# Kernel optimization log

Measured on AMD Instinct MI355X. Metric: run time of the kernel, lower is better.

Reference implementation:

```python
import jax, jax.numpy as jnp
import numpy as np

VOCAB, D, L, HEADS, MAX_T = 32000, 1024, 6, 16, 2048
HD = D // HEADS
DFF = 4 * D
B, T = 2, 2048
EPS = 1e-5


def setup_inputs() -> dict:
    key = jax.random.key(0)
    ks = jax.random.split(key, 16)
    s = 0.02
    return {
        "ids": jax.random.randint(ks[0], (B, T), 0, VOCAB, dtype=jnp.int32),
        "emb": jax.random.normal(ks[1], (VOCAB, D), jnp.float32) * s,
        "pos": jax.random.normal(ks[2], (MAX_T, D), jnp.float32) * s,
        "ln1_g": jnp.ones((L, D), jnp.float32),
        "ln1_b": jnp.zeros((L, D), jnp.float32),
        "ln2_g": jnp.ones((L, D), jnp.float32),
        "ln2_b": jnp.zeros((L, D), jnp.float32),
        "qkv_w": jax.random.normal(ks[3], (L, 3 * D, D), jnp.float32) * s,
        "out_w": jax.random.normal(ks[4], (L, D, D), jnp.float32) * s,
        "mlp_w1": jax.random.normal(ks[5], (L, DFF, D), jnp.float32) * s,
        "mlp_b1": jnp.zeros((L, DFF), jnp.float32),
        "mlp_w2": jax.random.normal(ks[6], (L, D, DFF), jnp.float32) * s,
        "mlp_b2": jnp.zeros((L, D), jnp.float32),
        "lnf_g": jnp.ones((D,), jnp.float32),
        "lnf_b": jnp.zeros((D,), jnp.float32),
    }


def layernorm(x, g, b):
    mu = jnp.mean(x, axis=-1, keepdims=True)
    var = jnp.mean(jnp.square(x - mu), axis=-1, keepdims=True)
    return (x - mu) * jax.lax.rsqrt(var + EPS) * g + b


def attention(x, qkv_w, out_w):
    b, t, d = x.shape
    qkv = jnp.einsum('btd,ed->bte', x, qkv_w)  # [B,T,3D]
    qkv = qkv.reshape(b, t, 3, HEADS, HD)
    q, k, v = qkv[:, :, 0], qkv[:, :, 1], qkv[:, :, 2]  # [B,T,H,hd]
    scale = HD ** -0.5
    scores = jnp.einsum('bqhd,bkhd->bhqk', q, k) * scale
    causal = jnp.tril(jnp.ones((t, t), dtype=bool))
    scores = jnp.where(causal, scores, -jnp.inf)
    attn = jax.nn.softmax(scores, axis=-1)
    o = jnp.einsum('bhqk,bkhd->bqhd', attn, v).reshape(b, t, d)
    return jnp.einsum('btd,ed->bte', o, out_w)


def reference(ids, emb, pos, ln1_g, ln1_b, ln2_g, ln2_b, qkv_w, out_w,
              mlp_w1, mlp_b1, mlp_w2, mlp_b2, lnf_g, lnf_b):
    t = ids.shape[1]
    x = emb[ids] + pos[:t][None, :, :]
    for l in range(L):
        x = x + attention(layernorm(x, ln1_g[l], ln1_b[l]), qkv_w[l], out_w[l])
        h = layernorm(x, ln2_g[l], ln2_b[l])
        h = jax.nn.gelu(jnp.einsum('btd,fd->btf', h, mlp_w1[l]) + mlp_b1[l], approximate=False)
        x = x + jnp.einsum('btf,df->btd', h, mlp_w2[l]) + mlp_b2[l]
    x = layernorm(x, lnf_g, lnf_b)
    return jnp.einsum('btd,vd->btv', x, emb)  # tied head
```

## Files before the change

kernel.cpp:

```cpp
#include <hip/hip_runtime.h>
#include <math.h>

#define TSEQ   2048
#define BATCH  2
#define DMODEL 1024
#define NLAYER 6
#define NHEAD  16
#define HDIM   64
#define DFFN   4096
#define NVOCAB 32000
#define LNEPS  1e-5f

typedef __bf16 bf16_t;
typedef bf16_t bf16x8 __attribute__((ext_vector_type(8)));
typedef float  f32x4  __attribute__((ext_vector_type(4)));
typedef unsigned short u16;
typedef u16 u16x4 __attribute__((ext_vector_type(4)));
typedef u16 u16x8 __attribute__((ext_vector_type(8)));

#define GBAR()   __builtin_amdgcn_s_barrier()
#define WLGKM0() asm volatile("s_waitcnt lgkmcnt(0)" ::: "memory")
#define WVM4()   asm volatile("s_waitcnt vmcnt(4)" ::: "memory")
#define WVM2()   asm volatile("s_waitcnt vmcnt(2)" ::: "memory")
#define WVM0()   asm volatile("s_waitcnt vmcnt(0)" ::: "memory")

__device__ __forceinline__ u16 f2bf(float f) {
  unsigned u = __float_as_uint(f);
  return (u16)((u + 0x7fffu + ((u >> 16) & 1u)) >> 16);
}

__device__ __forceinline__ void gload16(const void* g, void* l) {
  __builtin_amdgcn_global_load_lds(
      (const __attribute__((address_space(1))) unsigned int*)g,
      (__attribute__((address_space(3))) unsigned int*)l, 16, 0, 0);
}

__global__ __launch_bounds__(256) void embed_kernel(
    const int* __restrict__ ids, const float* __restrict__ emb,
    const float* __restrict__ pos, float* __restrict__ x) {
  int bt  = blockIdx.x;
  int t   = bt & (TSEQ - 1);
  int id  = ids[bt];
  int tid = threadIdx.x;
  float4 e = ((const float4*)(emb + (size_t)id * DMODEL))[tid];
  float4 p = ((const float4*)(pos + (size_t)t  * DMODEL))[tid];
  float4 r;
  r.x = e.x + p.x; r.y = e.y + p.y; r.z = e.z + p.z; r.w = e.w + p.w;
  ((float4*)(x + (size_t)bt * DMODEL))[tid] = r;
}

__device__ __forceinline__ void ln_body(
    const float* __restrict__ x, const float* __restrict__ g,
    const float* __restrict__ b, u16* __restrict__ y, int row, float* red) {
  int tid = threadIdx.x;
  int lane = tid & 63, w = tid >> 6;
  float4 v = ((const float4*)(x + (size_t)row * DMODEL))[tid];
  float s = v.x + v.y + v.z + v.w;
#pragma unroll
  for (int o = 32; o >= 1; o >>= 1) s += __shfl_xor(s, o);
  if (lane == 0) red[w] = s;
  __syncthreads();
  float mu = (red[0] + red[1] + red[2] + red[3]) * (1.0f / DMODEL);
  float d0 = v.x - mu, d1 = v.y - mu, d2 = v.z - mu, d3 = v.w - mu;
  float s2 = d0*d0 + d1*d1 + d2*d2 + d3*d3;
#pragma unroll
  for (int o = 32; o >= 1; o >>= 1) s2 += __shfl_xor(s2, o);
  if (lane == 0) red[4 + w] = s2;
  __syncthreads();
  float var = (red[4] + red[5] + red[6] + red[7]) * (1.0f / DMODEL);
  float rs = rsqrtf(var + LNEPS);
  float4 gv = ((const float4*)g)[tid];
  float4 bv = ((const float4*)b)[tid];
  u16x4 r;
  r[0] = f2bf(d0 * rs * gv.x + bv.x);
  r[1] = f2bf(d1 * rs * gv.y + bv.y);
  r[2] = f2bf(d2 * rs * gv.z + bv.z);
  r[3] = f2bf(d3 * rs * gv.w + bv.w);
  ((u16x4*)(y + (size_t)row * DMODEL))[tid] = r;
}

__global__ __launch_bounds__(256) void ln_kernel(
    const float* __restrict__ x, const float* __restrict__ g,
    const float* __restrict__ b, u16* __restrict__ y) {
  __shared__ float red[8];
  ln_body(x, g, b, y, blockIdx.x, red);
}

__device__ __forceinline__ void cvt8_body(const float* src, u16* dst, size_t i) {
  f32x4 a = __builtin_nontemporal_load((const f32x4*)(src + i));
  f32x4 b = __builtin_nontemporal_load((const f32x4*)(src + i) + 1);
  u16x8 r;
  r[0] = f2bf(a[0]); r[1] = f2bf(a[1]); r[2] = f2bf(a[2]); r[3] = f2bf(a[3]);
  r[4] = f2bf(b[0]); r[5] = f2bf(b[1]); r[6] = f2bf(b[2]); r[7] = f2bf(b[3]);
  *(u16x8*)(dst + i) = r;
}

__global__ __launch_bounds__(256) void prep_kernel(
    const float* __restrict__ s0, const float* __restrict__ s1,
    const float* __restrict__ s2, const float* __restrict__ s3,
    u16* __restrict__ d0, u16* __restrict__ d1,
    u16* __restrict__ d2, u16* __restrict__ d3,
    const float* __restrict__ x, const float* __restrict__ g,
    const float* __restrict__ b, u16* __restrict__ y) {
  __shared__ float red[8];
  int bid = blockIdx.x;
  if (bid >= 6144) {
    ln_body(x, g, b, y, bid - 6144, red);
    return;
  }
  const float* src; u16* dst; int idx;
  if (bid < 1536)      { src = s0; dst = d0; idx = bid; }
  else if (bid < 2048) { src = s1; dst = d1; idx = bid - 1536; }
  else if (bid < 4096) { src = s2; dst = d2; idx = bid - 2048; }
  else                 { src = s3; dst = d3; idx = bid - 4096; }
  cvt8_body(src, dst, ((size_t)idx * 256 + threadIdx.x) * 8);
}

__global__ __launch_bounds__(256) void finprep_kernel(
    const float* __restrict__ x, const float* __restrict__ g,
    const float* __restrict__ b, u16* __restrict__ y,
    const float* __restrict__ emb, u16* __restrict__ embb) {
  __shared__ float red[8];
  int bid = blockIdx.x;
  if (bid < 4096) {
    ln_body(x, g, b, y, bid, red);
    return;
  }
  cvt8_body(emb, embb, ((size_t)(bid - 4096) * 256 + threadIdx.x) * 8);
}

__device__ __forceinline__ float gelu_f(float v) {
  return 0.5f * v * (1.0f + erff(v * 0.70710678118654752f));
}

__device__ __forceinline__ bf16x8 ldsrd(const char* p) {
  return *(const bf16x8*)p;
}

template<int QD>
__device__ __forceinline__ void rd_a(bf16x8 (&afr)[2][2], const char* base,
                                     int aB0, int aB1) {
  afr[0][0] = ldsrd(base + aB0 + QD * 4096);
  afr[0][1] = ldsrd(base + aB1 + QD * 4096);
  afr[1][0] = ldsrd(base + aB0 + QD * 4096 + 2048);
  afr[1][1] = ldsrd(base + aB1 + QD * 4096 + 2048);
}

__device__ __forceinline__ void rd_b(bf16x8 (&bfr)[4][2], const char* base,
                                     int bB0, int bB1) {
#pragma unroll
  for (int ni = 0; ni < 4; ++ni) {
    bfr[ni][0] = ldsrd(base + bB0 + ni * 2048);
    bfr[ni][1] = ldsrd(base + bB1 + ni * 2048);
  }
}

template<int QD>
__device__ __forceinline__ void mm16(f32x4 (&acc)[8][4], bf16x8 (&afr)[2][2],
                                     bf16x8 (&bfr)[4][2]) {
#pragma unroll
  for (int ni = 0; ni < 4; ++ni) {
    acc[QD*2+0][ni] = __builtin_amdgcn_mfma_f32_16x16x32_bf16(bfr[ni][0], afr[0][0], acc[QD*2+0][ni], 0, 0, 0);
    acc[QD*2+0][ni] = __builtin_amdgcn_mfma_f32_16x16x32_bf16(bfr[ni][1], afr[0][1], acc[QD*2+0][ni], 0, 0, 0);
    acc[QD*2+1][ni] = __builtin_amdgcn_mfma_f32_16x16x32_bf16(bfr[ni][0], afr[1][0], acc[QD*2+1][ni], 0, 0, 0);
    acc[QD*2+1][ni] = __builtin_amdgcn_mfma_f32_16x16x32_bf16(bfr[ni][1], afr[1][1], acc[QD*2+1][ni], 0, 0, 0);
  }
}

template<int ACT, bool BIAS, bool OUTBF, bool NTB>
__global__ __launch_bounds__(512, 2) void gemm_mfma256(
    const bf16_t* __restrict__ A, const bf16_t* __restrict__ W,
    const float* __restrict__ bias, void* __restrict__ Cout,
    int M, int N, int K) {
  __shared__ char lds[131072];
  char* Asc = lds;
  char* Bsc = lds + 65536;

  const int tid  = threadIdx.x;
  const int lane = tid & 63;
  const int w    = tid >> 6;
  const int wr   = w >> 2, wc = w & 3;

  const int nwg = gridDim.x * gridDim.y;
  const int bid = blockIdx.y * gridDim.x + blockIdx.x;
  const int swz = (bid & 7) * (nwg >> 3) + (bid >> 3);
  const int m0 = (swz & 15) << 8;
  const int n0 = (swz >> 4) << 8;

  const size_t K2 = (size_t)K * 2;
  const int KT = K >> 6;

  const int qsrc = (((tid & 7) ^ ((tid >> 3) & 7)) << 4);
  const char* srcA = (const char*)A + (size_t)(m0 + (tid >> 3)) * K2 + qsrc;
  const char* srcB = (const char*)W + (size_t)(n0 + (tid >> 3)) * K2 + qsrc;
  char* dstA = Asc + (tid & 448) * 16;
  char* dstB = Bsc + (tid & 448) * 16;

  auto STG = [&](int kt, int part) {
    if (kt >= KT) return;
    const int h = part & 1;
    const size_t so = (size_t)(h * 128) * K2 + (size_t)kt * 128;
    const int dofs = ((kt & 1) << 15) + (h << 14);
    if (part >= 2) {
      gload16(srcA + so, dstA + dofs);
      gload16(srcA + so + 64 * K2, dstA + dofs + 8192);
    } else {
      gload16(srcB + so, dstB + dofs);
      gload16(srcB + so + 64 * K2, dstB + dofs + 8192);
    }
  };

  const int rr = lane & 15;
  const int q0 = (((lane >> 4) ^ (lane & 7)) << 4);
  const int aB0 = ((wr << 7) + rr) * 128 + q0;
  const int aB1 = ((wr << 7) + rr) * 128 + (q0 ^ 64);
  const int bB0 = ((wc << 6) + rr) * 128 + q0;
  const int bB1 = ((wc << 6) + rr) * 128 + (q0 ^ 64);

  bf16x8 bfr[4][2];
  bf16x8 afr[2][2];
  f32x4 acc[8][4] = {};

  STG(0, 0); STG(0, 1); STG(0, 2); STG(0, 3);
  STG(1, 0); STG(1, 1);
  WVM4();
  GBAR();

  const int iters = KT >> 1;
  for (int t = 0; t < iters; ++t) {
    const int d = t << 1;
    rd_b(bfr, Bsc, bB0, bB1);
    rd_a<0>(afr, Asc, aB0, aB1);
    STG(d + 1, 2); STG(d + 1, 3);
    GBAR(); WLGKM0();
    __builtin_amdgcn_s_setprio(1); mm16<0>(acc, afr, bfr); __builtin_amdgcn_s_setprio(0);
    GBAR();
    rd_a<1>(afr, Asc, aB0, aB1);
    STG(d + 2, 0);
    GBAR(); WLGKM0();
    __builtin_amdgcn_s_setprio(1); mm16<1>(acc, afr, bfr); __builtin_amdgcn_s_setprio(0);
    GBAR();
    rd_a<2>(afr, Asc, aB0, aB1);
    STG(d + 2, 1);
    GBAR(); WLGKM0();
    __builtin_amdgcn_s_setprio(1); mm16<2>(acc, afr, bfr); __builtin_amdgcn_s_setprio(0);
    GBAR();
    rd_a<3>(afr, Asc, aB0, aB1);
    GBAR(); WLGKM0();
    __builtin_amdgcn_s_setprio(1); mm16<3>(acc, afr, bfr); __builtin_amdgcn_s_setprio(0);
    if (t == iters - 1) { WVM0(); } else { WVM4(); }
    GBAR();
    rd_b(bfr, Bsc + 32768, bB0, bB1);
    rd_a<0>(afr, Asc + 32768, aB0, aB1);
    STG(d + 2, 2);
    GBAR(); WLGKM0();
    __builtin_amdgcn_s_setprio(1); mm16<0>(acc, afr, bfr); __builtin_amdgcn_s_setprio(0);
    GBAR();
    rd_a<1>(afr, Asc + 32768, aB0, aB1);
    STG(d + 2, 3);
    GBAR(); WLGKM0();
    __builtin_amdgcn_s_setprio(1); mm16<1>(acc, afr, bfr); __builtin_amdgcn_s_setprio(0);
    GBAR();
    rd_a<2>(afr, Asc + 32768, aB0, aB1);
    STG(d + 3, 0);
    GBAR(); WLGKM0();
    __builtin_amdgcn_s_setprio(1); mm16<2>(acc, afr, bfr); __builtin_amdgcn_s_setprio(0);
    GBAR();
    rd_a<3>(afr, Asc + 32768, aB0, aB1);
    STG(d + 3, 1);
    GBAR(); WLGKM0();
    __builtin_amdgcn_s_setprio(1); mm16<3>(acc, afr, bfr); __builtin_amdgcn_s_setprio(0);
    WVM4();
    GBAR();
  }

  const int cc = lane & 15;
  const int jb = (lane >> 4) << 2;

  if (NTB) {
    float* lbuf = (float*)lds;
#pragma unroll
    for (int h = 0; h < 2; ++h) {
      if (h) GBAR();
#pragma unroll
      for (int mi4 = 0; mi4 < 4; ++mi4) {
        const int lr = wr * 64 + mi4 * 16 + cc;
#pragma unroll
        for (int ni = 0; ni < 4; ++ni) {
          const int colb = (wc * 64 + ni * 16 + jb) * 4;
          f32x4 v = acc[h * 4 + mi4][ni];
          if (BIAS) v += *(const f32x4*)(bias + n0 + wc * 64 + ni * 16 + jb);
          if (ACT == 1) {
#pragma unroll
            for (int j = 0; j < 4; ++j) v[j] = gelu_f(v[j]);
          }
          *(f32x4*)((char*)lbuf + lr * 1024 + (colb ^ ((lr & 7) << 4))) = v;
        }
      }
      GBAR();
#pragma unroll
      for (int r = 0; r < 16; ++r) {
        const int lr = w * 16 + r;
        const int grow = m0 + h * 64 + lr + ((lr >> 6) << 6);
        const int cb = (lane * 16) ^ ((lr & 7) << 4);
        f32x4 v = *(const f32x4*)((const char*)lbuf + lr * 1024 + cb);
        __builtin_nontemporal_store(
            v, (f32x4*)((char*)((float*)Cout + (size_t)grow * N + n0) + lane * 16));
      }
    }
    return;
  }

  const int orow0 = m0 + wr * 128;
  const int ocol0 = n0 + wc * 64;
#pragma unroll
  for (int mi = 0; mi < 8; ++mi) {
    const int row = orow0 + mi * 16 + cc;
#pragma unroll
    for (int ni = 0; ni < 4; ++ni) {
      const int col = ocol0 + ni * 16 + jb;
      f32x4 v = acc[mi][ni];
      if (BIAS) v += *(const f32x4*)(bias + col);
      if (ACT == 1) {
#pragma unroll
        for (int j = 0; j < 4; ++j) v[j] = gelu_f(v[j]);
      }
      if (OUTBF) {
        u16x4 r;
#pragma unroll
        for (int j = 0; j < 4; ++j) r[j] = f2bf(v[j]);
        *(u16x4*)((u16*)Cout + (size_t)row * N + col) = r;
      } else {
        *(f32x4*)((float*)Cout + (size_t)row * N + col) = v;
      }
    }
  }
}

template<int PH>
__device__ __forceinline__ void rd_a2(bf16x8 (&afr)[2][2], const char* base,
                                      int aB0, int aB1) {
  afr[0][0] = ldsrd(base + aB0 + PH * 4096);
  afr[0][1] = ldsrd(base + aB1 + PH * 4096);
  afr[1][0] = ldsrd(base + aB0 + PH * 4096 + 2048);
  afr[1][1] = ldsrd(base + aB1 + PH * 4096 + 2048);
}

__device__ __forceinline__ void rd_b2(bf16x8 (&bfr)[2][2], const char* base,
                                      int bB0, int bB1) {
#pragma unroll
  for (int ni = 0; ni < 2; ++ni) {
    bfr[ni][0] = ldsrd(base + bB0 + ni * 2048);
    bfr[ni][1] = ldsrd(base + bB1 + ni * 2048);
  }
}

template<int PH>
__device__ __forceinline__ void mm8(f32x4 (&acc)[4][2], bf16x8 (&afr)[2][2],
                                    bf16x8 (&bfr)[2][2]) {
#pragma unroll
  for (int ni = 0; ni < 2; ++ni) {
    acc[PH*2+0][ni] = __builtin_amdgcn_mfma_f32_16x16x32_bf16(bfr[ni][0], afr[0][0], acc[PH*2+0][ni], 0, 0, 0);
    acc[PH*2+0][ni] = __builtin_amdgcn_mfma_f32_16x16x32_bf16(bfr[ni][1], afr[0][1], acc[PH*2+0][ni], 0, 0, 0);
    acc[PH*2+1][ni] = __builtin_amdgcn_mfma_f32_16x16x32_bf16(bfr[ni][0], afr[1][0], acc[PH*2+1][ni], 0, 0, 0);
    acc[PH*2+1][ni] = __builtin_amdgcn_mfma_f32_16x16x32_bf16(bfr[ni][1], afr[1][1], acc[PH*2+1][ni], 0, 0, 0);
  }
}

template<int ACT, bool BIAS, bool RES, bool OUTBF>
__global__ __launch_bounds__(512, 4) void gemm128_8ph(
    const bf16_t* __restrict__ A, const bf16_t* __restrict__ W,
    const float* __restrict__ bias, const float* __restrict__ res,
    void* __restrict__ Cout, int M, int N, int K) {
  __shared__ char lds[65536];
  char* Asc = lds;
  char* Bsc = lds + 32768;

  const int tid  = threadIdx.x;
  const int lane = tid & 63;
  const int w    = tid >> 6;
  const int wr   = w >> 2, wc = w & 3;

  const int nwg = gridDim.x * gridDim.y;
  const int bid = blockIdx.y * gridDim.x + blockIdx.x;
  const int swz = (bid & 7) * (nwg >> 3) + (bid >> 3);
  const int m0 = (swz & 31) << 7;
  const int n0 = (swz >> 5) << 7;

  const size_t K2 = (size_t)K * 2;
  const int KT = K >> 6;

  const int qsrc = (((tid & 7) ^ ((tid >> 3) & 7)) << 4);
  const char* srcA = (const char*)A + (size_t)(m0 + (tid >> 3)) * K2 + qsrc;
  const char* srcB = (const char*)W + (size_t)(n0 + (tid >> 3)) * K2 + qsrc;
  char* dstA = Asc + (tid & 448) * 16;
  char* dstB = Bsc + (tid & 448) * 16;

  auto STG = [&](int kt, int part) {
    if (kt >= KT) return;
    const int h = part & 1;
    const size_t so = (size_t)(h * 64) * K2 + (size_t)kt * 128;
    const int dofs = ((kt & 1) << 14) + (h << 13);
    if (part >= 2) gload16(srcA + so, dstA + dofs);
    else           gload16(srcB + so, dstB + dofs);
  };

  const int rr = lane & 15;
  const int q0 = (((lane >> 4) ^ (lane & 7)) << 4);
  const int aB0 = ((wr << 6) + rr) * 128 + q0;
  const int aB1 = ((wr << 6) + rr) * 128 + (q0 ^ 64);
  const int bB0 = ((wc << 5) + rr) * 128 + q0;
  const int bB1 = ((wc << 5) + rr) * 128 + (q0 ^ 64);

  bf16x8 bfr[2][2];
  bf16x8 afr[2][2];
  f32x4 acc[4][2] = {};

  STG(0, 0); STG(0, 1); STG(0, 2); STG(0, 3);
  STG(1, 0); STG(1, 1);
  WVM2();
  GBAR();

  const int iters = KT >> 1;
  for (int t = 0; t < iters; ++t) {
    const int d = t << 1;
    rd_b2(bfr, Bsc, bB0, bB1);
    rd_a2<0>(afr, Asc, aB0, aB1);
    STG(d + 1, 2); STG(d + 1, 3);
    GBAR(); WLGKM0();
    __builtin_amdgcn_s_setprio(1); mm8<0>(acc, afr, bfr); __builtin_amdgcn_s_setprio(0);
    GBAR();
    rd_a2<1>(afr, Asc, aB0, aB1);
    STG(d + 2, 0); STG(d + 2, 1);
    GBAR(); WLGKM0();
    __builtin_amdgcn_s_setprio(1); mm8<1>(acc, afr, bfr); __builtin_amdgcn_s_setprio(0);
    if (t == iters - 1) { WVM0(); } else { WVM2(); }
    GBAR();
    rd_b2(bfr, Bsc + 16384, bB0, bB1);
    rd_a2<0>(afr, Asc + 16384, aB0, aB1);
    STG(d + 2, 2); STG(d + 2, 3);
    GBAR(); WLGKM0();
    __builtin_amdgcn_s_setprio(1); mm8<0>(acc, afr, bfr); __builtin_amdgcn_s_setprio(0);
    GBAR();
    rd_a2<1>(afr, Asc + 16384, aB0, aB1);
    STG(d + 3, 0); STG(d + 3, 1);
    GBAR(); WLGKM0();
    __builtin_amdgcn_s_setprio(1); mm8<1>(acc, afr, bfr); __builtin_amdgcn_s_setprio(0);
    WVM2();
    GBAR();
  }

  const int cc = lane & 15;
  const int jb = (lane >> 4) << 2;
  const int orow0 = m0 + wr * 64;
  const int ocol0 = n0 + wc * 32;
#pragma unroll
  for (int mi = 0; mi < 4; ++mi) {
    const int row = orow0 + mi * 16 + cc;
#pragma unroll
    for (int ni = 0; ni < 2; ++ni) {
      const int col = ocol0 + ni * 16 + jb;
      f32x4 v = acc[mi][ni];
      if (BIAS) v += *(const f32x4*)(bias + col);
      if (ACT == 1) {
#pragma unroll
        for (int j = 0; j < 4; ++j) v[j] = gelu_f(v[j]);
      }
      if (RES) v += *(const f32x4*)(res + (size_t)row * N + col);
      if (OUTBF) {
        u16x4 r;
#pragma unroll
        for (int j = 0; j < 4; ++j) r[j] = f2bf(v[j]);
        *(u16x4*)((u16*)Cout + (size_t)row * N + col) = r;
      } else {
        *(f32x4*)((float*)Cout + (size_t)row * N + col) = v;
      }
    }
  }
}

__global__ __launch_bounds__(256) void attn_mfma_kernel(
    const u16* __restrict__ qkv, u16* __restrict__ out) {
  const int bh  = blockIdx.y;
  const int b = bh >> 4, h = bh & 15;
  const int tid = threadIdx.x;
  const int lane = tid & 63, w = tid >> 6;

  __shared__ u16 Ks[128][72];
  __shared__ u16 Vt[64][136];
  __shared__ u16 Ps[4][16][136];

  const size_t rowstr = 3 * DMODEL;
  const u16* base = qkv + (size_t)b * TSEQ * rowstr;

  const int fr = lane & 15;
  const int fk = (lane >> 4) * 8;

  bf16x8 onesf;
#pragma unroll
  for (int i = 0; i < 8; ++i) ((u16*)&onesf)[i] = 0x3F80;

  const int skr = tid >> 1;
  const int skc = (tid & 1) * 32;
  const int vk0 = (tid & 63) * 2;
  const int vd0 = (tid >> 6) * 16;

#pragma unroll 1
  for (int half = 0; half < 2; ++half) {
    const int qt  = half ? (31 - (int)blockIdx.x) : (int)blockIdx.x;
    const int qb0 = qt * 64;
    const int qminw = qb0 + w * 16;
    const int qrow = qminw + fr;

    u16x8 q0r = *(const u16x8*)(base + (size_t)qrow * rowstr + h * HDIM + fk);
    u16x8 q1r = *(const u16x8*)(base + (size_t)qrow * rowstr + h * HDIM + fk + 32);
    bf16x8 qf0, qf1;
#pragma unroll
    for (int i = 0; i < 8; ++i) {
      ((u16*)&qf0)[i] = f2bf(__uint_as_float((unsigned)q0r[i] << 16) * 0.125f);
      ((u16*)&qf1)[i] = f2bf(__uint_as_float((unsigned)q1r[i] << 16) * 0.125f);
    }

    f32x4 o[4] = {};
    f32x4 ls = {};

    u16x8 k0, k1, k2, k3, va0, va1, vb0, vb1;
    {
      const u16* kr = base + (size_t)skr * rowstr + DMODEL + h * HDIM + skc;
      k0 = *(const u16x8*)kr;        k1 = *(const u16x8*)(kr + 8);
      k2 = *(const u16x8*)(kr + 16); k3 = *(const u16x8*)(kr + 24);
      const u16* vr = base + (size_t)vk0 * rowstr + 2 * DMODEL + h * HDIM + vd0;
      va0 = *(const u16x8*)vr;            va1 = *(const u16x8*)(vr + 8);
      vb0 = *(const u16x8*)(vr + rowstr); vb1 = *(const u16x8*)(vr + rowstr + 8);
    }

    for (int s0 = 0; s0 < qb0 + 64; s0 += 128) {
      __syncthreads();
      *(u16x8*)&Ks[skr][skc]      = k0;
      *(u16x8*)&Ks[skr][skc + 8]  = k1;
      *(u16x8*)&Ks[skr][skc + 16] = k2;
      *(u16x8*)&Ks[skr][skc + 24] = k3;
#pragma unroll
      for (int i = 0; i < 8; ++i) {
        *(unsigned*)&Vt[vd0 + i][vk0]     = (unsigned)va0[i] | ((unsigned)vb0[i] << 16);
        *(unsigned*)&Vt[vd0 + 8 + i][vk0] = (unsigned)va1[i] | ((unsigned)vb1[i] << 16);
      }
      __syncthreads();

      if (s0 + 128 < qb0 + 64) {
        const u16* kr = base + (size_t)(s0 + 128 + skr) * rowstr + DMODEL + h * HDIM + skc;
        k0 = *(const u16x8*)kr;        k1 = *(const u16x8*)(kr + 8);
        k2 = *(const u16x8*)(kr + 16); k3 = *(const u16x8*)(kr + 24);
        const u16* vr = base + (size_t)(s0 + 128 + vk0) * rowstr + 2 * DMODEL + h * HDIM + vd0;
        va0 = *(const u16x8*)vr;            va1 = *(const u16x8*)(vr + 8);
        vb0 = *(const u16x8*)(vr + rowstr); vb1 = *(const u16x8*)(vr + rowstr + 8);
      } else if (half == 0) {
        const u16* kr = base + (size_t)skr * rowstr + DMODEL + h * HDIM + skc;
        k0 = *(const u16x8*)kr;        k1 = *(const u16x8*)(kr + 8);
        k2 = *(const u16x8*)(kr + 16); k3 = *(const u16x8*)(kr + 24);
        const u16* vr = base + (size_t)vk0 * rowstr + 2 * DMODEL + h * HDIM + vd0;
        va0 = *(const u16x8*)vr;            va1 = *(const u16x8*)(vr + 8);
        vb0 = *(const u16x8*)(vr + rowstr); vb1 = *(const u16x8*)(vr + rowstr + 8);
      }

      const bool h2 = s0 < qb0;
      const int nl = h2 ? 8 : 4;

      f32x4 s[8];
      __builtin_amdgcn_s_setprio(1);
#pragma unroll
      for (int ni = 0; ni < 4; ++ni) {
        f32x4 t = {};
        bf16x8 kf0 = *(const bf16x8*)&Ks[ni * 16 + fr][fk];
        bf16x8 kf1 = *(const bf16x8*)&Ks[ni * 16 + fr][fk + 32];
        t = __builtin_amdgcn_mfma_f32_16x16x32_bf16(qf0, kf0, t, 0, 0, 0);
        t = __builtin_amdgcn_mfma_f32_16x16x32_bf16(qf1, kf1, t, 0, 0, 0);
        s[ni] = t;
      }
      __builtin_amdgcn_s_setprio(0);
      if (h2) {
        __builtin_amdgcn_s_setprio(1);
#pragma unroll
        for (int ni = 4; ni < 8; ++ni) {
          f32x4 t = {};
          bf16x8 kf0 = *(const bf16x8*)&Ks[ni * 16 + fr][fk];
          bf16x8 kf1 = *(const bf16x8*)&Ks[ni * 16 + fr][fk + 32];
          t = __builtin_amdgcn_mfma_f32_16x16x32_bf16(qf0, kf0, t, 0, 0, 0);
          t = __builtin_amdgcn_mfma_f32_16x16x32_bf16(qf1, kf1, t, 0, 0, 0);
          s[ni] = t;
        }
        __builtin_amdgcn_s_setprio(0);
      }

      if (s0 + 127 > qb0) {
        const int q0_ = qminw + (lane >> 4) * 4;
#pragma unroll
        for (int ni = 0; ni < 8; ++ni) {
          if (ni >= nl) break;
#pragma unroll
          for (int j = 0; j < 4; ++j)
            if (s0 + ni * 16 + fr > q0_ + j) s[ni][j] = -3e38f;
        }
      }

#pragma unroll
      for (int ni = 0; ni < 8; ++ni) {
        if (ni >= nl) break;
#pragma unroll
        for (int j = 0; j < 4; ++j) {
          float pv = __expf(fminf(s[ni][j], 80.f) - 8.f);
          Ps[w][(lane >> 4) * 4 + j][ni * 16 + fr] = f2bf(pv);
        }
      }
      WLGKM0();

      bf16x8 pf0 = *(const bf16x8*)&Ps[w][fr][fk];
      bf16x8 pf1 = *(const bf16x8*)&Ps[w][fr][fk + 32];
      __builtin_amdgcn_s_setprio(1);
#pragma unroll
      for (int ni = 0; ni < 4; ++ni) {
        bf16x8 vf0 = *(const bf16x8*)&Vt[ni * 16 + fr][fk];
        bf16x8 vf1 = *(const bf16x8*)&Vt[ni * 16 + fr][fk + 32];
        o[ni] = __builtin_amdgcn_mfma_f32_16x16x32_bf16(pf0, vf0, o[ni], 0, 0, 0);
        o[ni] = __builtin_amdgcn_mfma_f32_16x16x32_bf16(pf1, vf1, o[ni], 0, 0, 0);
      }
      ls = __builtin_amdgcn_mfma_f32_16x16x32_bf16(pf0, onesf, ls, 0, 0, 0);
      ls = __builtin_amdgcn_mfma_f32_16x16x32_bf16(pf1, onesf, ls, 0, 0, 0);
      __builtin_amdgcn_s_setprio(0);
      if (h2) {
        bf16x8 pf2 = *(const bf16x8*)&Ps[w][fr][64 + fk];
        bf16x8 pf3 = *(const bf16x8*)&Ps[w][fr][96 + fk];
        __builtin_amdgcn_s_setprio(1);
#pragma unroll
        for (int ni = 0; ni < 4; ++ni) {
          bf16x8 vf2 = *(const bf16x8*)&Vt[ni * 16 + fr][64 + fk];
          bf16x8 vf3 = *(const bf16x8*)&Vt[ni * 16 + fr][96 + fk];
          o[ni] = __builtin_amdgcn_mfma_f32_16x16x32_bf16(pf2, vf2, o[ni], 0, 0, 0);
          o[ni] = __builtin_amdgcn_mfma_f32_16x16x32_bf16(pf3, vf3, o[ni], 0, 0, 0);
        }
        ls = __builtin_amdgcn_mfma_f32_16x16x32_bf16(pf2, onesf, ls, 0, 0, 0);
        ls = __builtin_amdgcn_mfma_f32_16x16x32_bf16(pf3, onesf, ls, 0, 0, 0);
        __builtin_amdgcn_s_setprio(0);
      }
    }

#pragma unroll
    for (int j = 0; j < 4; ++j) {
      float inv = 1.0f / ls[j];
      int q = qminw + (lane >> 4) * 4 + j;
      u16* op = out + ((size_t)(b * TSEQ) + q) * DMODEL + h * HDIM + fr;
#pragma unroll
      for (int ni = 0; ni < 4; ++ni)
        op[ni * 16] = f2bf(o[ni][j] * inv);
    }
  }
}

extern "C" void kernel_launch(void* const* d_in, const int* in_sizes, int n_in,
                              void* d_out, int out_size, void* d_ws, size_t ws_size,
                              hipStream_t stream) {
  const int*   ids    = (const int*)d_in[0];
  const float* emb    = (const float*)d_in[1];
  const float* pos    = (const float*)d_in[2];
  const float* ln1_g  = (const float*)d_in[3];
  const float* ln1_b  = (const float*)d_in[4];
  const float* ln2_g  = (const float*)d_in[5];
  const float* ln2_b  = (const float*)d_in[6];
  const float* qkv_w  = (const float*)d_in[7];
  const float* out_w  = (const float*)d_in[8];
  const float* mlp_w1 = (const float*)d_in[9];
  const float* mlp_b1 = (const float*)d_in[10];
  const float* mlp_w2 = (const float*)d_in[11];
  const float* mlp_b2 = (const float*)d_in[12];
  const float* lnf_g  = (const float*)d_in[13];
  const float* lnf_b  = (const float*)d_in[14];
  float* outp = (float*)d_out;

  const int M = BATCH * TSEQ;
  char* p = (char*)d_ws;
  float* x    = (float*)p;  p += (size_t)M * DMODEL * 4;
  u16*   yb   = (u16*)p;    p += (size_t)M * DMODEL * 2;
  u16*   qkvb = (u16*)p;    p += (size_t)M * 3 * DMODEL * 2;
  u16*   mid  = (u16*)p;    p += (size_t)M * DFFN * 2;
  u16*   wq   = (u16*)p;    p += (size_t)3 * DMODEL * DMODEL * 2;
  u16*   wo   = (u16*)p;    p += (size_t)DMODEL * DMODEL * 2;
  u16*   w1   = (u16*)p;    p += (size_t)DFFN * DMODEL * 2;
  u16*   w2   = (u16*)p;    p += (size_t)DMODEL * DFFN * 2;
  u16*   embb = qkvb;

  embed_kernel<<<M, 256, 0, stream>>>(ids, emb, pos, x);

  for (int l = 0; l < NLAYER; ++l) {
    prep_kernel<<<10240, 256, 0, stream>>>(
        qkv_w  + (size_t)l * 3 * DMODEL * DMODEL,
        out_w  + (size_t)l * DMODEL * DMODEL,
        mlp_w1 + (size_t)l * DFFN * DMODEL,
        mlp_w2 + (size_t)l * DMODEL * DFFN,
        wq, wo, w1, w2,
        x, ln1_g + l * DMODEL, ln1_b + l * DMODEL, yb);

    gemm_mfma256<0, false, true, false><<<dim3(3 * DMODEL / 256, M / 256), 512, 0, stream>>>(
        (const bf16_t*)yb, (const bf16_t*)wq, nullptr, qkvb, M, 3 * DMODEL, DMODEL);
    attn_mfma_kernel<<<dim3(16, BATCH * NHEAD), 256, 0, stream>>>(qkvb, yb);
    gemm128_8ph<0, false, true, false><<<dim3(DMODEL / 128, M / 128), 512, 0, stream>>>(
        (const bf16_t*)yb, (const bf16_t*)wo, nullptr, x, x, M, DMODEL, DMODEL);
    ln_kernel<<<M, 256, 0, stream>>>(x, ln2_g + l * DMODEL, ln2_b + l * DMODEL, yb);
    gemm_mfma256<1, true, true, false><<<dim3(DFFN / 256, M / 256), 512, 0, stream>>>(
        (const bf16_t*)yb, (const bf16_t*)w1, mlp_b1 + (size_t)l * DFFN, mid,
        M, DFFN, DMODEL);
    gemm128_8ph<0, true, true, false><<<dim3(DMODEL / 128, M / 128), 512, 0, stream>>>(
        (const bf16_t*)mid, (const bf16_t*)w2, mlp_b2 + (size_t)l * DMODEL, x, x,
        M, DMODEL, DFFN);
  }

  finprep_kernel<<<20096, 256, 0, stream>>>(x, lnf_g, lnf_b, yb, emb, embb);
  gemm_mfma256<0, false, false, true><<<dim3(NVOCAB / 256, M / 256), 512, 0, stream>>>(
      (const bf16_t*)yb, (const bf16_t*)embb, nullptr, outp, M, NVOCAB, DMODEL);
}
```

Before: 1.715 ms.

## Widen attention blocks to 128 query rows and use 128-tile GEMM for QKV

```diff
diff --git a/kernel.cpp b/kernel.cpp
--- a/kernel.cpp
+++ b/kernel.cpp
@@ -27,6 +27,12 @@
 __device__ __forceinline__ u16 f2bf(float f) {
   unsigned u = __float_as_uint(f);
   return (u16)((u + 0x7fffu + ((u >> 16) & 1u)) >> 16);
+}
+
+__device__ __forceinline__ float exp2_raw(float x) {
+  float r;
+  asm("v_exp_f32 %0, %1" : "=v"(r) : "v"(x));
+  return r;
 }
 
 __device__ __forceinline__ void gload16(const void* g, void* l) {
@@ -479,7 +485,7 @@
   }
 }
 
-__global__ __launch_bounds__(256) void attn_mfma_kernel(
+__global__ __launch_bounds__(512) void attn_mfma_kernel(
     const u16* __restrict__ qkv, u16* __restrict__ out) {
   const int bh  = blockIdx.y;
   const int b = bh >> 4, h = bh & 15;
@@ -488,7 +494,7 @@
 
   __shared__ u16 Ks[128][72];
   __shared__ u16 Vt[64][136];
-  __shared__ u16 Ps[4][16][136];
+  __shared__ u16 Ps[8][16][136];
 
   const size_t rowstr = 3 * DMODEL;
   const u16* base = qkv + (size_t)b * TSEQ * rowstr;
@@ -500,15 +506,15 @@
 #pragma unroll
   for (int i = 0; i < 8; ++i) ((u16*)&onesf)[i] = 0x3F80;
 
-  const int skr = tid >> 1;
-  const int skc = (tid & 1) * 32;
+  const int skr = tid >> 2;
+  const int skc = (tid & 3) * 16;
   const int vk0 = (tid & 63) * 2;
-  const int vd0 = (tid >> 6) * 16;
+  const int vd0 = (tid >> 6) * 8;
 
 #pragma unroll 1
   for (int half = 0; half < 2; ++half) {
-    const int qt  = half ? (31 - (int)blockIdx.x) : (int)blockIdx.x;
-    const int qb0 = qt * 64;
+    const int st  = half ? (15 - (int)blockIdx.x) : (int)blockIdx.x;
+    const int qb0 = st * 128;
     const int qminw = qb0 + w * 16;
     const int qrow = qminw + fr;
 
@@ -517,59 +523,46 @@
     bf16x8 qf0, qf1;
 #pragma unroll
     for (int i = 0; i < 8; ++i) {
-      ((u16*)&qf0)[i] = f2bf(__uint_as_float((unsigned)q0r[i] << 16) * 0.125f);
-      ((u16*)&qf1)[i] = f2bf(__uint_as_float((unsigned)q1r[i] << 16) * 0.125f);
+      ((u16*)&qf0)[i] = f2bf(__uint_as_float((unsigned)q0r[i] << 16) * 0.18033688011112042f);
+      ((u16*)&qf1)[i] = f2bf(__uint_as_float((unsigned)q1r[i] << 16) * 0.18033688011112042f);
     }
 
     f32x4 o[4] = {};
     f32x4 ls = {};
 
-    u16x8 k0, k1, k2, k3, va0, va1, vb0, vb1;
+    u16x8 k0, k1, va0, vb0;
     {
       const u16* kr = base + (size_t)skr * rowstr + DMODEL + h * HDIM + skc;
-      k0 = *(const u16x8*)kr;        k1 = *(const u16x8*)(kr + 8);
-      k2 = *(const u16x8*)(kr + 16); k3 = *(const u16x8*)(kr + 24);
+      k0 = *(const u16x8*)kr;  k1 = *(const u16x8*)(kr + 8);
       const u16* vr = base + (size_t)vk0 * rowstr + 2 * DMODEL + h * HDIM + vd0;
-      va0 = *(const u16x8*)vr;            va1 = *(const u16x8*)(vr + 8);
-      vb0 = *(const u16x8*)(vr + rowstr); vb1 = *(const u16x8*)(vr + rowstr + 8);
-    }
-
-    for (int s0 = 0; s0 < qb0 + 64; s0 += 128) {
+      va0 = *(const u16x8*)vr; vb0 = *(const u16x8*)(vr + rowstr);
+    }
+
+    for (int s0 = 0; s0 < qb0 + 128; s0 += 128) {
       __syncthreads();
-      *(u16x8*)&Ks[skr][skc]      = k0;
-      *(u16x8*)&Ks[skr][skc + 8]  = k1;
-      *(u16x8*)&Ks[skr][skc + 16] = k2;
-      *(u16x8*)&Ks[skr][skc + 24] = k3;
-#pragma unroll
-      for (int i = 0; i < 8; ++i) {
-        *(unsigned*)&Vt[vd0 + i][vk0]     = (unsigned)va0[i] | ((unsigned)vb0[i] << 16);
-        *(unsigned*)&Vt[vd0 + 8 + i][vk0] = (unsigned)va1[i] | ((unsigned)vb1[i] << 16);
-      }
+      *(u16x8*)&Ks[skr][skc]     = k0;
+      *(u16x8*)&Ks[skr][skc + 8] = k1;
+#pragma unroll
+      for (int i = 0; i < 8; ++i)
+        *(unsigned*)&Vt[vd0 + i][vk0] = (unsigned)va0[i] | ((unsigned)vb0[i] << 16);
       __syncthreads();
 
-      if (s0 + 128 < qb0 + 64) {
+      if (s0 + 128 < qb0 + 128) {
         const u16* kr = base + (size_t)(s0 + 128 + skr) * rowstr + DMODEL + h * HDIM + skc;
-        k0 = *(const u16x8*)kr;        k1 = *(const u16x8*)(kr + 8);
-        k2 = *(const u16x8*)(kr + 16); k3 = *(const u16x8*)(kr + 24);
+        k0 = *(const u16x8*)kr;  k1 = *(const u16x8*)(kr + 8);
         const u16* vr = base + (size_t)(s0 + 128 + vk0) * rowstr + 2 * DMODEL + h * HDIM + vd0;
-        va0 = *(const u16x8*)vr;            va1 = *(const u16x8*)(vr + 8);
-        vb0 = *(const u16x8*)(vr + rowstr); vb1 = *(const u16x8*)(vr + rowstr + 8);
+        va0 = *(const u16x8*)vr; vb0 = *(const u16x8*)(vr + rowstr);
       } else if (half == 0) {
         const u16* kr = base + (size_t)skr * rowstr + DMODEL + h * HDIM + skc;
-        k0 = *(const u16x8*)kr;        k1 = *(const u16x8*)(kr + 8);
-        k2 = *(const u16x8*)(kr + 16); k3 = *(const u16x8*)(kr + 24);
+        k0 = *(const u16x8*)kr;  k1 = *(const u16x8*)(kr + 8);
         const u16* vr = base + (size_t)vk0 * rowstr + 2 * DMODEL + h * HDIM + vd0;
-        va0 = *(const u16x8*)vr;            va1 = *(const u16x8*)(vr + 8);
-        vb0 = *(const u16x8*)(vr + rowstr); vb1 = *(const u16x8*)(vr + rowstr + 8);
-      }
-
-      const bool h2 = s0 < qb0;
-      const int nl = h2 ? 8 : 4;
+        va0 = *(const u16x8*)vr; vb0 = *(const u16x8*)(vr + rowstr);
+      }
 
       f32x4 s[8];
       __builtin_amdgcn_s_setprio(1);
 #pragma unroll
-      for (int ni = 0; ni < 4; ++ni) {
+      for (int ni = 0; ni < 8; ++ni) {
         f32x4 t = {};
         bf16x8 kf0 = *(const bf16x8*)&Ks[ni * 16 + fr][fk];
         bf16x8 kf1 = *(const bf16x8*)&Ks[ni * 16 + fr][fk + 32];
@@ -578,70 +571,46 @@
         s[ni] = t;
       }
       __builtin_amdgcn_s_setprio(0);
-      if (h2) {
-        __builtin_amdgcn_s_setprio(1);
-#pragma unroll
-        for (int ni = 4; ni < 8; ++ni) {
-          f32x4 t = {};
-          bf16x8 kf0 = *(const bf16x8*)&Ks[ni * 16 + fr][fk];
-          bf16x8 kf1 = *(const bf16x8*)&Ks[ni * 16 + fr][fk + 32];
-          t = __builtin_amdgcn_mfma_f32_16x16x32_bf16(qf0, kf0, t, 0, 0, 0);
-          t = __builtin_amdgcn_mfma_f32_16x16x32_bf16(qf1, kf1, t, 0, 0, 0);
-          s[ni] = t;
-        }
-        __builtin_amdgcn_s_setprio(0);
-      }
-
-      if (s0 + 127 > qb0) {
+
+      if (s0 == qb0) {
         const int q0_ = qminw + (lane >> 4) * 4;
 #pragma unroll
-        for (int ni = 0; ni < 8; ++ni) {
-          if (ni >= nl) break;
+        for (int ni = 0; ni < 8; ++ni)
 #pragma unroll
           for (int j = 0; j < 4; ++j)
             if (s0 + ni * 16 + fr > q0_ + j) s[ni][j] = -3e38f;
-        }
-      }
-
-#pragma unroll
-      for (int ni = 0; ni < 8; ++ni) {
-        if (ni >= nl) break;
+      }
+
+#pragma unroll
+      for (int ni = 0; ni < 8; ++ni)
 #pragma unroll
         for (int j = 0; j < 4; ++j) {
-          float pv = __expf(fminf(s[ni][j], 80.f) - 8.f);
+          float pv = exp2_raw(fminf(s[ni][j], 115.41560327f) - 11.541560327111707f);
           Ps[w][(lane >> 4) * 4 + j][ni * 16 + fr] = f2bf(pv);
         }
-      }
       WLGKM0();
 
       bf16x8 pf0 = *(const bf16x8*)&Ps[w][fr][fk];
       bf16x8 pf1 = *(const bf16x8*)&Ps[w][fr][fk + 32];
+      bf16x8 pf2 = *(const bf16x8*)&Ps[w][fr][64 + fk];
+      bf16x8 pf3 = *(const bf16x8*)&Ps[w][fr][96 + fk];
       __builtin_amdgcn_s_setprio(1);
 #pragma unroll
       for (int ni = 0; ni < 4; ++ni) {
         bf16x8 vf0 = *(const bf16x8*)&Vt[ni * 16 + fr][fk];
         bf16x8 vf1 = *(const bf16x8*)&Vt[ni * 16 + fr][fk + 32];
+        bf16x8 vf2 = *(const bf16x8*)&Vt[ni * 16 + fr][64 + fk];
+        bf16x8 vf3 = *(const bf16x8*)&Vt[ni * 16 + fr][96 + fk];
         o[ni] = __builtin_amdgcn_mfma_f32_16x16x32_bf16(pf0, vf0, o[ni], 0, 0, 0);
         o[ni] = __builtin_amdgcn_mfma_f32_16x16x32_bf16(pf1, vf1, o[ni], 0, 0, 0);
+        o[ni] = __builtin_amdgcn_mfma_f32_16x16x32_bf16(pf2, vf2, o[ni], 0, 0, 0);
+        o[ni] = __builtin_amdgcn_mfma_f32_16x16x32_bf16(pf3, vf3, o[ni], 0, 0, 0);
       }
       ls = __builtin_amdgcn_mfma_f32_16x16x32_bf16(pf0, onesf, ls, 0, 0, 0);
       ls = __builtin_amdgcn_mfma_f32_16x16x32_bf16(pf1, onesf, ls, 0, 0, 0);
+      ls = __builtin_amdgcn_mfma_f32_16x16x32_bf16(pf2, onesf, ls, 0, 0, 0);
+      ls = __builtin_amdgcn_mfma_f32_16x16x32_bf16(pf3, onesf, ls, 0, 0, 0);
       __builtin_amdgcn_s_setprio(0);
-      if (h2) {
-        bf16x8 pf2 = *(const bf16x8*)&Ps[w][fr][64 + fk];
-        bf16x8 pf3 = *(const bf16x8*)&Ps[w][fr][96 + fk];
-        __builtin_amdgcn_s_setprio(1);
-#pragma unroll
-        for (int ni = 0; ni < 4; ++ni) {
-          bf16x8 vf2 = *(const bf16x8*)&Vt[ni * 16 + fr][64 + fk];
-          bf16x8 vf3 = *(const bf16x8*)&Vt[ni * 16 + fr][96 + fk];
-          o[ni] = __builtin_amdgcn_mfma_f32_16x16x32_bf16(pf2, vf2, o[ni], 0, 0, 0);
-          o[ni] = __builtin_amdgcn_mfma_f32_16x16x32_bf16(pf3, vf3, o[ni], 0, 0, 0);
-        }
-        ls = __builtin_amdgcn_mfma_f32_16x16x32_bf16(pf2, onesf, ls, 0, 0, 0);
-        ls = __builtin_amdgcn_mfma_f32_16x16x32_bf16(pf3, onesf, ls, 0, 0, 0);
-        __builtin_amdgcn_s_setprio(0);
-      }
     }
 
 #pragma unroll
@@ -699,9 +668,9 @@
         wq, wo, w1, w2,
         x, ln1_g + l * DMODEL, ln1_b + l * DMODEL, yb);
 
-    gemm_mfma256<0, false, true, false><<<dim3(3 * DMODEL / 256, M / 256), 512, 0, stream>>>(
-        (const bf16_t*)yb, (const bf16_t*)wq, nullptr, qkvb, M, 3 * DMODEL, DMODEL);
-    attn_mfma_kernel<<<dim3(16, BATCH * NHEAD), 256, 0, stream>>>(qkvb, yb);
+    gemm128_8ph<0, false, false, true><<<dim3(3 * DMODEL / 128, M / 128), 512, 0, stream>>>(
+        (const bf16_t*)yb, (const bf16_t*)wq, nullptr, nullptr, qkvb, M, 3 * DMODEL, DMODEL);
+    attn_mfma_kernel<<<dim3(8, BATCH * NHEAD), 512, 0, stream>>>(qkvb, yb);
     gemm128_8ph<0, false, true, false><<<dim3(DMODEL / 128, M / 128), 512, 0, stream>>>(
         (const bf16_t*)yb, (const bf16_t*)wo, nullptr, x, x, M, DMODEL, DMODEL);
     ln_kernel<<<M, 256, 0, stream>>>(x, ln2_g + l * DMODEL, ln2_b + l * DMODEL, yb);
```

Result: faster. 1.618 ms (-5.7%).
